# Performance work log

Hardware: AMD Instinct MI355X
Metric: run time of the kernel (lower is better)

The kernel has to match this reference:

```python
import jax, jax.numpy as jnp
import numpy as np

EPS = 1e-06
K = 16  # instance ids 1..K
W_IOU, W_VAR, W_SEED = 1.0, 10.0, 1.0


def _lovasz_hinge_flat(logits, labels):
    # logits, labels: (N,) flat; labels in {0,1}
    signs = 2.0 * labels - 1.0
    errors = 1.0 - logits * signs
    perm = jnp.argsort(-errors)  # descending
    errors_sorted = errors[perm]
    gt_sorted = labels[perm]
    gts = gt_sorted.sum()
    intersection = gts - jnp.cumsum(gt_sorted)
    union = gts + jnp.cumsum(1.0 - gt_sorted)
    jaccard = 1.0 - intersection / jnp.maximum(union, 1e-08)
    jaccard = jnp.concatenate([jaccard[:1], jaccard[1:] - jaccard[:-1]])
    return jnp.dot(jax.nn.relu(errors_sorted), jaccard)


def _forward(y_pred, y_true):
    B, C, H, W = y_pred.shape
    D = 2
    off = y_pred[:, :D]              # (B,D,H,W)
    sig = y_pred[:, D:2 * D]         # (B,D,H,W)
    seed = y_pred[:, 2 * D]          # (B,H,W)
    dt = y_pred.dtype

    gy, gx = jnp.meshgrid(jnp.arange(H, dtype=dt), jnp.arange(W, dtype=dt), indexing='ij')
    grid = jnp.stack([gy, gx])       # (D,H,W)
    emb = grid[None] + off           # (B,D,H,W)

    ids = jnp.arange(1, K + 1)
    mask = (y_true[:, None] == ids[None, :, None, None]).astype(dt)  # (B,K,H,W)
    count = mask.sum((2, 3))                                         # (B,K)
    safe = jnp.maximum(count, 1.0)
    present = (count > 0).astype(dt)
    n_present = jnp.maximum(present.sum(), 1.0)

    # per-instance embedding centers
    Ck = jnp.einsum('bkhw,bdhw->bkd', mask, emb) / safe[..., None]   # (B,K,D)
    sb = jnp.maximum(sig, EPS)                                       # (B,D,H,W)
    diff = emb[:, None] - Ck[..., None, None]                        # (B,K,D,H,W)
    quad = diff * diff / (2.0 * sb[:, None] ** 2)
    phi = jnp.clip(jnp.exp(-quad.sum(2)), EPS, 1.0 - EPS)            # (B,K,H,W)
    logits = jnp.log(phi) - jnp.log1p(-phi)

    lov = jax.vmap(_lovasz_hinge_flat)(logits.reshape(B * K, -1), mask.reshape(B * K, -1))
    L_iou = (lov * present.reshape(-1)).sum() / n_present

    # sigma smoothness: mean over instances of mean_{d,pixels in mask}|sig - mean_k(sig)|
    mean_sig = jnp.einsum('bkhw,bdhw->bkd', mask, sig) / safe[..., None]  # (B,K,D)
    dev = (jnp.abs(sig[:, None] - mean_sig[..., None, None]) * mask[:, :, None]).sum((2, 3, 4))
    dev = dev / (D * safe)                                           # (B,K)
    L_var = (dev * present).sum() / n_present

    seed_target = (phi * mask).sum(1)                                # (B,H,W)
    L_seed = jnp.mean((seed - seed_target) ** 2)

    return W_IOU * L_iou + W_VAR * L_var + W_SEED * L_seed


def setup_inputs() -> dict:
    key = jax.random.key(0)
    k1, k2 = jax.random.split(key)
    B, H, W = 4, 768, 768
    y_pred = jax.random.uniform(k1, (B, 5, H, W), dtype=jnp.float32)
    y_true = jax.random.randint(k2, (B, H, W), 0, K + 1)
    return {"y_pred": y_pred, "y_true": y_true}


def reference(y_pred, y_true):
    return _forward(y_pred, y_true)
```

## Files before the change

kernel.cpp:

```cpp
#include <hip/hip_runtime.h>

typedef float f32x2 __attribute__((ext_vector_type(2)));

#define HWPIX 589824
#define Wdim 768
#define Bdim 4
#define Kdim 16
#define NBINS 2048
#define RANGE_F 16.0f
#define BIN_W (RANGE_F / NBINS)
#define INV_BIN_W (NBINS / RANGE_F)
#define EPSf 1e-6f
#define QCLIP 13.8155106f

#define Q4 (HWPIX / 4)

#define NSB_S 192
#define GPI_S (NSB_S * 256)
#define NTHREADS_S (NSB_S * Bdim * 256)
#define NSB_M 288
#define GPI_M (NSB_M * 256)

#define ACC_OFF 0
#define LOVARR_OFF 724
#define HIST_OFF_F 1024
#define NHIST (Bdim * Kdim * 2 * NBINS)
#define POSNH_OFF_F (HIST_OFF_F + NHIST)
#define SPART_OFF (POSNH_OFF_F + 64)
#define MPART_OFF (SPART_OFF + Bdim * NSB_S * 80)

__global__ __launch_bounds__(256, 3) void k_stats(const float* __restrict__ yp,
                                                  const int* __restrict__ yt,
                                                  float* __restrict__ ws,
                                                  unsigned* __restrict__ hist) {
    int b = blockIdx.y;
    int lane = threadIdx.x & 63;
    int wv = threadIdx.x >> 6;
    __shared__ float lpart[4][80];

    {
        int gtid = (blockIdx.y * NSB_S + blockIdx.x) * 256 + threadIdx.x;
        for (int i = gtid; i < NHIST + 64; i += NTHREADS_S) hist[i] = 0u;
    }

    const float4* bp4 = (const float4*)(yp + (size_t)b * 5 * HWPIX);
    const int4* bt4 = (const int4*)(yt + (size_t)b * HWPIX);

    f32x2 acc2[40];
#pragma unroll
    for (int v = 0; v < 40; ++v) acc2[v] = (f32x2){0.f, 0.f};

    for (int p = 0; p < 3; ++p) {
        int g = p * GPI_S + blockIdx.x * 256 + threadIdx.x;
        float4 voy = bp4[g];
        float4 vox = bp4[g + Q4];
        float4 vsy = bp4[g + 2 * Q4];
        float4 vsx = bp4[g + 3 * Q4];
        int4 vt = bt4[g];
        int hwb = g * 4;
        float oy[4] = {voy.x, voy.y, voy.z, voy.w};
        float ox[4] = {vox.x, vox.y, vox.z, vox.w};
        float sy[4] = {vsy.x, vsy.y, vsy.z, vsy.w};
        float sx[4] = {vsx.x, vsx.y, vsx.z, vsx.w};
        int tt[4] = {vt.x, vt.y, vt.z, vt.w};
#pragma unroll
        for (int j = 0; j < 4; ++j) {
            int hw = hwb + j;
            int h = hw / Wdim;
            int w = hw - h * Wdim;
            int own = tt[j] - 1;
            float vy = (float)h + oy[j];
            float vx = (float)w + ox[j];
#pragma unroll
            for (int q = 0; q < 8; ++q) {
                f32x2 m2 = {(own == 2 * q) ? 1.0f : 0.0f,
                            (own == 2 * q + 1) ? 1.0f : 0.0f};
                acc2[q * 5 + 0] += m2;
                acc2[q * 5 + 1] += m2 * vy;
                acc2[q * 5 + 2] += m2 * vx;
                acc2[q * 5 + 3] += m2 * sy[j];
                acc2[q * 5 + 4] += m2 * sx[j];
            }
        }
    }

#define ACCV(v) (acc2[((v) / 5 / 2) * 5 + (v) % 5][((v) / 5) & 1])

    bool lo = (lane < 32);
#pragma unroll
    for (int v = 0; v < 40; ++v) {
        float send = lo ? ACCV(v + 40) : ACCV(v);
        float got = __shfl_xor(send, 32);
        ACCV(v) += lo ? got : 0.f;
        ACCV(v + 40) += lo ? 0.f : got;
    }
#pragma unroll
    for (int v = 0; v < 40; ++v) {
        float x = lo ? ACCV(v) : ACCV(v + 40);
#pragma unroll
        for (int o = 16; o >= 1; o >>= 1) x += __shfl_xor(x, o);
        if ((lane & 31) == 0) lpart[wv][lo ? v : v + 40] = x;
    }
    __syncthreads();
    if (threadIdx.x < 80) {
        float v = lpart[0][threadIdx.x] + lpart[1][threadIdx.x] +
                  lpart[2][threadIdx.x] + lpart[3][threadIdx.x];
        ws[SPART_OFF + (size_t)(b * NSB_S + blockIdx.x) * 80 + threadIdx.x] = v;
    }
#undef ACCV
}

__global__ void k_centers2(float* __restrict__ ws) {
    int wv = threadIdx.x >> 6;
    int lane = threadIdx.x & 63;
    int gw = blockIdx.x * 4 + wv;
    int b = gw / 80, idx = gw - b * 80;
    const float* sp = ws + SPART_OFF + (size_t)b * NSB_S * 80 + idx;
    float x = sp[(size_t)lane * 80] + sp[(size_t)(lane + 64) * 80] +
              sp[(size_t)(lane + 128) * 80];
#pragma unroll
    for (int o = 32; o >= 1; o >>= 1) x += __shfl_xor(x, o);
    if (lane == 0) ws[ACC_OFF + b * 80 + idx] = x;
}

__global__ __launch_bounds__(256, 4) void k_main(const float* __restrict__ yp,
                                                 const int* __restrict__ yt,
                                                 float* __restrict__ ws,
                                                 unsigned* __restrict__ hist) {
    int b = blockIdx.y;
    int lane = threadIdx.x & 63;
    int wv = threadIdx.x >> 6;
    __shared__ float ck_s[32];
    __shared__ float4 msw_s[17];
    __shared__ float part[4][2];
    if (threadIdx.x < 16) {
        int k = threadIdx.x;
        const float* a = ws + ACC_OFF + (size_t)b * 80 + k * 5;
        float cnt = a[0];
        float safe = fmaxf(cnt, 1.0f);
        float inv = 1.0f / safe;
        ck_s[k * 2 + 0] = a[1] * inv;
        ck_s[k * 2 + 1] = a[2] * inv;
        float4 mw;
        mw.x = a[3] * inv;
        mw.y = a[4] * inv;
        mw.z = (cnt > 0.f) ? 0.5f / cnt : 0.f;
        mw.w = 0.f;
        msw_s[k] = mw;
    }
    if (threadIdx.x == 16) msw_s[16] = (float4){0.f, 0.f, 0.f, 0.f};
    __syncthreads();

    f32x2 cky2[8], ckx2[8];
#pragma unroll
    for (int q = 0; q < 8; ++q) {
        cky2[q] = (f32x2){ck_s[4 * q], ck_s[4 * q + 2]};
        ckx2[q] = (f32x2){ck_s[4 * q + 1], ck_s[4 * q + 3]};
    }

    unsigned* hb = hist + (size_t)(b * Kdim) * 2 * NBINS;
    unsigned* posnh = hist + (size_t)NHIST;
    const float4* bp4 = (const float4*)(yp + (size_t)b * 5 * HWPIX);
    const int4* bt4 = (const int4*)(yt + (size_t)b * HWPIX);

    float varsum = 0.f, ssum = 0.f;
    for (int p = 0; p < 2; ++p) {
        int g = p * GPI_M + blockIdx.x * 256 + threadIdx.x;
        float4 voy = bp4[g];
        float4 vox = bp4[g + Q4];
        float4 vsy = bp4[g + 2 * Q4];
        float4 vsx = bp4[g + 3 * Q4];
        float4 vse = bp4[g + 4 * Q4];
        int4 vt = bt4[g];
        int hwb = g * 4;
        float oy[4] = {voy.x, voy.y, voy.z, voy.w};
        float ox[4] = {vox.x, vox.y, vox.z, vox.w};
        float sya[4] = {vsy.x, vsy.y, vsy.z, vsy.w};
        float sxa[4] = {vsx.x, vsx.y, vsx.z, vsx.w};
        float sea[4] = {vse.x, vse.y, vse.z, vse.w};
        int tt[4] = {vt.x, vt.y, vt.z, vt.w};
#pragma unroll
        for (int j = 0; j < 4; ++j) {
            int hw = hwb + j;
            int h = hw / Wdim;
            int w = hw - h * Wdim;
            int own = tt[j] - 1;
            float sy = sya[j], sx = sxa[j];
            float ey = (float)h + oy[j], ex = (float)w + ox[j];
            float sby = fmaxf(sy, EPSf), sbx = fmaxf(sx, EPSf);
            float iy = 0.5f / (sby * sby), ix = 0.5f / (sbx * sbx);

            unsigned sm = 0;
#pragma unroll
            for (int q = 0; q < 8; ++q) {
                f32x2 dy2 = ey - cky2[q];
                f32x2 dx2 = ex - ckx2[q];
                f32x2 q2 = dy2 * dy2 * iy + dx2 * dx2 * ix;
                if (q2.x < QCLIP) sm |= (1u << (2 * q));
                if (q2.y < QCLIP) sm |= (1u << (2 * q + 1));
            }
            int ow = (own >= 0) ? own : 16;
            float4 mw = msw_s[ow];
            float devv = fabsf(sy - mw.x) + fabsf(sx - mw.y);
            varsum = fmaf(devv, mw.z, varsum);

            float st = (own >= 0) ? EPSf : 0.f;
            while (sm) {
                int k = __ffs(sm) - 1;
                sm &= sm - 1;
                float dy = ey - ck_s[k * 2];
                float dx = ex - ck_s[k * 2 + 1];
                float q = fmaf(dy * dy, iy, dx * dx * ix);
                float phi = expf(-q);
                phi = fminf(fmaxf(phi, EPSf), 1.0f - EPSf);
                float lg = logf(phi) - log1pf(-phi);
                bool isPos = (k == own);
                float e;
                if (isPos) {
                    st = phi;
                    atomicAdd(&posnh[b * Kdim + k], 1u);
                    e = 1.0f - lg;
                } else {
                    e = 1.0f + lg;
                }
                if (e > 0.f) {
                    int bin = (int)(e * INV_BIN_W);
                    if (bin > NBINS - 1) bin = NBINS - 1;
                    atomicAdd(&hb[(k * 2 + (isPos ? 1 : 0)) * NBINS + bin], 1u);
                }
            }
            float dd = sea[j] - st;
            ssum = fmaf(dd, dd, ssum);
        }
    }
#pragma unroll
    for (int o = 32; o >= 1; o >>= 1) {
        varsum += __shfl_xor(varsum, o);
        ssum += __shfl_xor(ssum, o);
    }
    if (lane == 0) {
        part[wv][0] = varsum;
        part[wv][1] = ssum;
    }
    __syncthreads();
    if (threadIdx.x < 2) {
        float v = part[0][threadIdx.x] + part[1][threadIdx.x] +
                  part[2][threadIdx.x] + part[3][threadIdx.x];
        ws[MPART_OFF + (size_t)(b * NSB_M + blockIdx.x) * 2 + threadIdx.x] = v;
    }
}

__global__ void k_lovasz(float* __restrict__ ws, const unsigned* __restrict__ hist) {
    int i = blockIdx.x;
    int lane = threadIdx.x;
    float P = ws[ACC_OFF + i * 5];
    if (P < 0.5f) {
        if (lane == 0) ws[LOVARR_OFF + i] = 0.f;
        return;
    }
    const unsigned* hn = hist + (size_t)i * 2 * NBINS;
    const unsigned* hp = hn + NBINS;
    const unsigned* posnh = hist + (size_t)NHIST;
    const float C_LO = logf(EPSf) - log1pf(-EPSf);
    const int HOTBIN = (int)((1.0f - C_LO) * INV_BIN_W);
    int deficit = (int)(P + 0.5f) - (int)posnh[i];
    int carry_p = 0, carry_n = 0;
    float Jtop = 0.f;
    float trap = 0.f;
    for (int c = NBINS / 64 - 1; c >= 0; --c) {
        int m = c * 64 + lane;
        int vp = (int)hp[m];
        int vn = (int)hn[m];
        if (m == HOTBIN) vp += deficit;
        for (int o = 1; o < 64; o <<= 1) {
            int tp = __shfl_down(vp, o);
            int tn = __shfl_down(vn, o);
            if (lane + o < 64) { vp += tp; vn += tn; }
        }
        float p_edge = (float)(carry_p + vp);
        float n_edge = (float)(carry_n + vn);
        float J = 1.0f - (P - p_edge) / (P + n_edge);
        float Jn = __shfl_down(J, 1);
        if (lane == 63) Jn = Jtop;
        trap += 0.5f * (J + Jn);
        carry_p += __shfl(vp, 0);
        carry_n += __shfl(vn, 0);
        Jtop = __shfl(J, 0);
    }
    for (int o = 1; o < 64; o <<= 1) {
        float t2 = __shfl_down(trap, o);
        if (lane + o < 64) trap += t2;
    }
    if (lane == 0) ws[LOVARR_OFF + i] = trap * BIN_W;
}

__global__ void k_final(const float* __restrict__ ws, float* __restrict__ out) {
    __shared__ float r0[256], r1[256], r2[256], r3[256];
    int t = threadIdx.x;
    float v = 0.f, s = 0.f, l = 0.f, pr = 0.f;
    for (int j = t; j < Bdim * NSB_M; j += 256) {
        v += ws[MPART_OFF + 2 * j];
        s += ws[MPART_OFF + 2 * j + 1];
    }
    if (t < 64) {
        l = ws[LOVARR_OFF + t];
        pr = (ws[ACC_OFF + t * 5] > 0.f) ? 1.f : 0.f;
    }
    r0[t] = v; r1[t] = s; r2[t] = l; r3[t] = pr;
    __syncthreads();
    for (int o = 128; o > 0; o >>= 1) {
        if (t < o) {
            r0[t] += r0[t + o]; r1[t] += r1[t + o];
            r2[t] += r2[t + o]; r3[t] += r3[t + o];
        }
        __syncthreads();
    }
    if (t == 0) {
        float npres = fmaxf(r3[0], 1.0f);
        out[0] = r2[0] / npres + 10.0f * (r0[0] / npres) +
                 r1[0] / (float)((size_t)Bdim * HWPIX);
    }
}

extern "C" void kernel_launch(void* const* d_in, const int* in_sizes, int n_in,
                              void* d_out, int out_size, void* d_ws, size_t ws_size,
                              hipStream_t stream) {
    const float* yp = (const float*)d_in[0];
    const int* yt = (const int*)d_in[1];
    float* ws = (float*)d_ws;
    unsigned* hist = (unsigned*)((char*)d_ws + HIST_OFF_F * 4);

    dim3 gs(NSB_S, Bdim);
    dim3 gm(NSB_M, Bdim);
    k_stats<<<gs, 256, 0, stream>>>(yp, yt, ws, hist);
    k_centers2<<<80, 256, 0, stream>>>(ws);
    k_main<<<gm, 256, 0, stream>>>(yp, yt, ws, hist);
    k_lovasz<<<64, 64, 0, stream>>>(ws, hist);
    k_final<<<1, 256, 0, stream>>>(ws, (float*)d_out);
}
```

Before: 83.26 us.

## Fuse stats, centers, main and Lovasz kernels into one cooperative kernel

Merges the four separate kernel launches into one cooperative kernel that uses grid-wide syncs between phases. The main phase's grid shrinks from 288 to 192 blocks per batch, each doing three iterations, and the Lovasz phase now packs four instances per 256-thread block. This is meant to remove launch gaps and inter-kernel drain time. The cost is grid-sync overhead, and it relies on 768 blocks fitting co-resident; if the cooperative launch fails it falls back to four ordinary launches.

```diff
diff --git a/kernel.cpp b/kernel.cpp
--- a/kernel.cpp
+++ b/kernel.cpp
@@ -1,4 +1,7 @@
 #include <hip/hip_runtime.h>
+#include <hip/hip_cooperative_groups.h>
+
+namespace cg = cooperative_groups;
 
 typedef float f32x2 __attribute__((ext_vector_type(2)));
 
@@ -14,44 +17,37 @@
 #define QCLIP 13.8155106f
 
 #define Q4 (HWPIX / 4)
-
-#define NSB_S 192
-#define GPI_S (NSB_S * 256)
-#define NTHREADS_S (NSB_S * Bdim * 256)
-#define NSB_M 288
-#define GPI_M (NSB_M * 256)
+#define NBLK 768
+#define NSB 192
+#define GPI (NSB * 256)
 
 #define ACC_OFF 0
 #define LOVARR_OFF 724
 #define HIST_OFF_F 1024
 #define NHIST (Bdim * Kdim * 2 * NBINS)
-#define POSNH_OFF_F (HIST_OFF_F + NHIST)
-#define SPART_OFF (POSNH_OFF_F + 64)
-#define MPART_OFF (SPART_OFF + Bdim * NSB_S * 80)
-
-__global__ __launch_bounds__(256, 3) void k_stats(const float* __restrict__ yp,
-                                                  const int* __restrict__ yt,
-                                                  float* __restrict__ ws,
-                                                  unsigned* __restrict__ hist) {
-    int b = blockIdx.y;
-    int lane = threadIdx.x & 63;
-    int wv = threadIdx.x >> 6;
+#define SPART_OFF (HIST_OFF_F + NHIST + 64)
+#define MPART_OFF (SPART_OFF + NBLK * 80)
+
+
+__device__ __forceinline__ void phaseA(const float* __restrict__ yp,
+                                       const int* __restrict__ yt,
+                                       float* __restrict__ ws,
+                                       unsigned* __restrict__ hist,
+                                       int blk, int tid) {
+    int lane = tid & 63, wv = tid >> 6;
     __shared__ float lpart[4][80];
-
-    {
-        int gtid = (blockIdx.y * NSB_S + blockIdx.x) * 256 + threadIdx.x;
-        for (int i = gtid; i < NHIST + 64; i += NTHREADS_S) hist[i] = 0u;
-    }
-
+    int b = blk / NSB, xblk = blk - b * NSB;
     const float4* bp4 = (const float4*)(yp + (size_t)b * 5 * HWPIX);
     const int4* bt4 = (const int4*)(yt + (size_t)b * HWPIX);
 
+    for (int i = blk * 256 + tid; i < NHIST + 64; i += NBLK * 256) hist[i] = 0u;
+
     f32x2 acc2[40];
 #pragma unroll
     for (int v = 0; v < 40; ++v) acc2[v] = (f32x2){0.f, 0.f};
 
     for (int p = 0; p < 3; ++p) {
-        int g = p * GPI_S + blockIdx.x * 256 + threadIdx.x;
+        int g = p * GPI + xblk * 256 + tid;
         float4 voy = bp4[g];
         float4 vox = bp4[g + Q4];
         float4 vsy = bp4[g + 2 * Q4];
@@ -85,7 +81,6 @@
     }
 
 #define ACCV(v) (acc2[((v) / 5 / 2) * 5 + (v) % 5][((v) / 5) & 1])
-
     bool lo = (lane < 32);
 #pragma unroll
     for (int v = 0; v < 40; ++v) {
@@ -101,40 +96,42 @@
         for (int o = 16; o >= 1; o >>= 1) x += __shfl_xor(x, o);
         if ((lane & 31) == 0) lpart[wv][lo ? v : v + 40] = x;
     }
+#undef ACCV
     __syncthreads();
-    if (threadIdx.x < 80) {
-        float v = lpart[0][threadIdx.x] + lpart[1][threadIdx.x] +
-                  lpart[2][threadIdx.x] + lpart[3][threadIdx.x];
-        ws[SPART_OFF + (size_t)(b * NSB_S + blockIdx.x) * 80 + threadIdx.x] = v;
-    }
-#undef ACCV
-}
-
-__global__ void k_centers2(float* __restrict__ ws) {
-    int wv = threadIdx.x >> 6;
-    int lane = threadIdx.x & 63;
-    int gw = blockIdx.x * 4 + wv;
-    int b = gw / 80, idx = gw - b * 80;
-    const float* sp = ws + SPART_OFF + (size_t)b * NSB_S * 80 + idx;
+    if (tid < 80) {
+        float v = lpart[0][tid] + lpart[1][tid] + lpart[2][tid] + lpart[3][tid];
+        ws[SPART_OFF + (size_t)blk * 80 + tid] = v;
+    }
+}
+
+__device__ __forceinline__ void phaseB(float* __restrict__ ws, int blk, int tid) {
+    if (blk >= 80) return;
+    int wv = tid >> 6, lane = tid & 63;
+    int gw = blk * 4 + wv;
+    int bb = gw / 80, idx = gw - bb * 80;
+    const float* sp = ws + SPART_OFF + (size_t)bb * NSB * 80 + idx;
     float x = sp[(size_t)lane * 80] + sp[(size_t)(lane + 64) * 80] +
               sp[(size_t)(lane + 128) * 80];
 #pragma unroll
     for (int o = 32; o >= 1; o >>= 1) x += __shfl_xor(x, o);
-    if (lane == 0) ws[ACC_OFF + b * 80 + idx] = x;
-}
-
-__global__ __launch_bounds__(256, 4) void k_main(const float* __restrict__ yp,
-                                                 const int* __restrict__ yt,
-                                                 float* __restrict__ ws,
-                                                 unsigned* __restrict__ hist) {
-    int b = blockIdx.y;
-    int lane = threadIdx.x & 63;
-    int wv = threadIdx.x >> 6;
+    if (lane == 0) ws[ACC_OFF + bb * 80 + idx] = x;
+}
+
+__device__ __forceinline__ void phaseC(const float* __restrict__ yp,
+                                       const int* __restrict__ yt,
+                                       float* __restrict__ ws,
+                                       unsigned* __restrict__ hist,
+                                       int blk, int tid) {
+    int lane = tid & 63, wv = tid >> 6;
     __shared__ float ck_s[32];
     __shared__ float4 msw_s[17];
     __shared__ float part[4][2];
-    if (threadIdx.x < 16) {
-        int k = threadIdx.x;
+    int b = blk / NSB, xblk = blk - b * NSB;
+    const float4* bp4 = (const float4*)(yp + (size_t)b * 5 * HWPIX);
+    const int4* bt4 = (const int4*)(yt + (size_t)b * HWPIX);
+
+    if (tid < 16) {
+        int k = tid;
         const float* a = ws + ACC_OFF + (size_t)b * 80 + k * 5;
         float cnt = a[0];
         float safe = fmaxf(cnt, 1.0f);
@@ -148,7 +145,7 @@
         mw.w = 0.f;
         msw_s[k] = mw;
     }
-    if (threadIdx.x == 16) msw_s[16] = (float4){0.f, 0.f, 0.f, 0.f};
+    if (tid == 16) msw_s[16] = (float4){0.f, 0.f, 0.f, 0.f};
     __syncthreads();
 
     f32x2 cky2[8], ckx2[8];
@@ -160,12 +157,10 @@
 
     unsigned* hb = hist + (size_t)(b * Kdim) * 2 * NBINS;
     unsigned* posnh = hist + (size_t)NHIST;
-    const float4* bp4 = (const float4*)(yp + (size_t)b * 5 * HWPIX);
-    const int4* bt4 = (const int4*)(yt + (size_t)b * HWPIX);
 
     float varsum = 0.f, ssum = 0.f;
-    for (int p = 0; p < 2; ++p) {
-        int g = p * GPI_M + blockIdx.x * 256 + threadIdx.x;
+    for (int p = 0; p < 3; ++p) {
+        int g = p * GPI + xblk * 256 + tid;
         float4 voy = bp4[g];
         float4 vox = bp4[g + Q4];
         float4 vsy = bp4[g + 2 * Q4];
@@ -243,62 +238,100 @@
         part[wv][1] = ssum;
     }
     __syncthreads();
-    if (threadIdx.x < 2) {
-        float v = part[0][threadIdx.x] + part[1][threadIdx.x] +
-                  part[2][threadIdx.x] + part[3][threadIdx.x];
-        ws[MPART_OFF + (size_t)(b * NSB_M + blockIdx.x) * 2 + threadIdx.x] = v;
-    }
-}
-
-__global__ void k_lovasz(float* __restrict__ ws, const unsigned* __restrict__ hist) {
-    int i = blockIdx.x;
-    int lane = threadIdx.x;
+    if (tid < 2) {
+        float v = part[0][tid] + part[1][tid] + part[2][tid] + part[3][tid];
+        ws[MPART_OFF + (size_t)blk * 2 + tid] = v;
+    }
+}
+
+__device__ __forceinline__ void phaseD(float* __restrict__ ws,
+                                       const unsigned* __restrict__ hist,
+                                       int blk, int tid) {
+    if (blk >= 16) return;
+    int wv = tid >> 6, lane = tid & 63;
+    int i = blk * 4 + wv;
     float P = ws[ACC_OFF + i * 5];
-    if (P < 0.5f) {
-        if (lane == 0) ws[LOVARR_OFF + i] = 0.f;
-        return;
-    }
-    const unsigned* hn = hist + (size_t)i * 2 * NBINS;
-    const unsigned* hp = hn + NBINS;
-    const unsigned* posnh = hist + (size_t)NHIST;
-    const float C_LO = logf(EPSf) - log1pf(-EPSf);
-    const int HOTBIN = (int)((1.0f - C_LO) * INV_BIN_W);
-    int deficit = (int)(P + 0.5f) - (int)posnh[i];
-    int carry_p = 0, carry_n = 0;
-    float Jtop = 0.f;
-    float trap = 0.f;
-    for (int c = NBINS / 64 - 1; c >= 0; --c) {
-        int m = c * 64 + lane;
-        int vp = (int)hp[m];
-        int vn = (int)hn[m];
-        if (m == HOTBIN) vp += deficit;
+    float res = 0.f;
+    if (P >= 0.5f) {
+        const unsigned* hn = hist + (size_t)i * 2 * NBINS;
+        const unsigned* hp = hn + NBINS;
+        const unsigned* posnh = hist + (size_t)NHIST;
+        const float C_LO = logf(EPSf) - log1pf(-EPSf);
+        const int HOTBIN = (int)((1.0f - C_LO) * INV_BIN_W);
+        int deficit = (int)(P + 0.5f) - (int)posnh[i];
+        int carry_p = 0, carry_n = 0;
+        float Jtop = 0.f;
+        float trap = 0.f;
+        for (int c = NBINS / 64 - 1; c >= 0; --c) {
+            int m = c * 64 + lane;
+            int vp = (int)hp[m];
+            int vn = (int)hn[m];
+            if (m == HOTBIN) vp += deficit;
+            for (int o = 1; o < 64; o <<= 1) {
+                int tp = __shfl_down(vp, o);
+                int tn = __shfl_down(vn, o);
+                if (lane + o < 64) { vp += tp; vn += tn; }
+            }
+            float p_edge = (float)(carry_p + vp);
+            float n_edge = (float)(carry_n + vn);
+            float J = 1.0f - (P - p_edge) / (P + n_edge);
+            float Jn = __shfl_down(J, 1);
+            if (lane == 63) Jn = Jtop;
+            trap += 0.5f * (J + Jn);
+            carry_p += __shfl(vp, 0);
+            carry_n += __shfl(vn, 0);
+            Jtop = __shfl(J, 0);
+        }
         for (int o = 1; o < 64; o <<= 1) {
-            int tp = __shfl_down(vp, o);
-            int tn = __shfl_down(vn, o);
-            if (lane + o < 64) { vp += tp; vn += tn; }
-        }
-        float p_edge = (float)(carry_p + vp);
-        float n_edge = (float)(carry_n + vn);
-        float J = 1.0f - (P - p_edge) / (P + n_edge);
-        float Jn = __shfl_down(J, 1);
-        if (lane == 63) Jn = Jtop;
-        trap += 0.5f * (J + Jn);
-        carry_p += __shfl(vp, 0);
-        carry_n += __shfl(vn, 0);
-        Jtop = __shfl(J, 0);
-    }
-    for (int o = 1; o < 64; o <<= 1) {
-        float t2 = __shfl_down(trap, o);
-        if (lane + o < 64) trap += t2;
-    }
-    if (lane == 0) ws[LOVARR_OFF + i] = trap * BIN_W;
+            float t2 = __shfl_down(trap, o);
+            if (lane + o < 64) trap += t2;
+        }
+        res = trap * BIN_W;
+    }
+    if (lane == 0) ws[LOVARR_OFF + i] = res;
+}
+
+
+__global__ __launch_bounds__(256, 3) void k_all(const float* __restrict__ yp,
+                                                const int* __restrict__ yt,
+                                                float* __restrict__ ws,
+                                                unsigned* __restrict__ hist) {
+    cg::grid_group grid = cg::this_grid();
+    int blk = blockIdx.x, tid = threadIdx.x;
+    phaseA(yp, yt, ws, hist, blk, tid);
+    grid.sync();
+    phaseB(ws, blk, tid);
+    grid.sync();
+    phaseC(yp, yt, ws, hist, blk, tid);
+    grid.sync();
+    phaseD(ws, hist, blk, tid);
+}
+
+
+__global__ __launch_bounds__(256, 3) void kA(const float* __restrict__ yp,
+                                             const int* __restrict__ yt,
+                                             float* __restrict__ ws,
+                                             unsigned* __restrict__ hist) {
+    phaseA(yp, yt, ws, hist, blockIdx.x, threadIdx.x);
+}
+__global__ void kB(float* __restrict__ ws) {
+    phaseB(ws, blockIdx.x, threadIdx.x);
+}
+__global__ __launch_bounds__(256, 3) void kC(const float* __restrict__ yp,
+                                             const int* __restrict__ yt,
+                                             float* __restrict__ ws,
+                                             unsigned* __restrict__ hist) {
+    phaseC(yp, yt, ws, hist, blockIdx.x, threadIdx.x);
+}
+__global__ void kD(float* __restrict__ ws, const unsigned* __restrict__ hist) {
+    phaseD(ws, hist, blockIdx.x, threadIdx.x);
 }
 
 __global__ void k_final(const float* __restrict__ ws, float* __restrict__ out) {
     __shared__ float r0[256], r1[256], r2[256], r3[256];
     int t = threadIdx.x;
     float v = 0.f, s = 0.f, l = 0.f, pr = 0.f;
-    for (int j = t; j < Bdim * NSB_M; j += 256) {
+    for (int j = t; j < NBLK; j += 256) {
         v += ws[MPART_OFF + 2 * j];
         s += ws[MPART_OFF + 2 * j + 1];
     }
@@ -330,11 +363,15 @@
     float* ws = (float*)d_ws;
     unsigned* hist = (unsigned*)((char*)d_ws + HIST_OFF_F * 4);
 
-    dim3 gs(NSB_S, Bdim);
-    dim3 gm(NSB_M, Bdim);
-    k_stats<<<gs, 256, 0, stream>>>(yp, yt, ws, hist);
-    k_centers2<<<80, 256, 0, stream>>>(ws);
-    k_main<<<gm, 256, 0, stream>>>(yp, yt, ws, hist);
-    k_lovasz<<<64, 64, 0, stream>>>(ws, hist);
+    void* args[4] = {(void*)&yp, (void*)&yt, (void*)&ws, (void*)&hist};
+    hipError_t err = hipLaunchCooperativeKernel((const void*)k_all, dim3(NBLK),
+                                                dim3(256), args, 0, stream);
+    if (err != hipSuccess) {
+        (void)hipGetLastError();
+        kA<<<dim3(NBLK), 256, 0, stream>>>(yp, yt, ws, hist);
+        kB<<<dim3(80), 256, 0, stream>>>(ws);
+        kC<<<dim3(NBLK), 256, 0, stream>>>(yp, yt, ws, hist);
+        kD<<<dim3(16), 256, 0, stream>>>(ws, hist);
+    }
     k_final<<<1, 256, 0, stream>>>(ws, (float*)d_out);
 }
```

Result: slower. 275.9 us (+231.4%).
